# Optimization experiments

Hardware: AMD Instinct MI355X
Metric: run time of the kernel (lower is better)

## Reference

```python
import math
import jax, jax.numpy as jnp
import numpy as np

D_MODEL = 1024
D_HIDDEN = 2048
N_EXPERTS = 8
TOP_K = 2
CAPACITY_FACTOR = 1.25


def setup_inputs() -> dict:
    key = jax.random.key(0)
    k0, k1, k2, k3 = jax.random.split(key, 4)
    B, T = 2, 2048
    x = jax.random.normal(k0, (B, T, D_MODEL), dtype=jnp.float32)
    # torch nn.Linear stores weight as [out_features, in_features]
    w_router = jax.random.normal(k1, (N_EXPERTS, D_MODEL), dtype=jnp.float32) * 0.02
    w_gate = jax.random.normal(k2, (D_HIDDEN, D_MODEL), dtype=jnp.float32) * 0.02
    w_down = jax.random.normal(k3, (N_EXPERTS, D_MODEL, D_HIDDEN), dtype=jnp.float32) * 0.02
    return {"x": x, "w_router": w_router, "w_gate": w_gate, "w_down": w_down}


def _moe_forward(x, w_router, w_gate, w_down):
    B, T, D = x.shape
    N = B * T
    xf = x.reshape(N, D)

    # Router (computed in fp32, as in the original)
    logits = xf.astype(jnp.float32) @ w_router.T            # [N, E]
    gates = jax.nn.softmax(logits, axis=-1)                  # [N, E]
    topk_gates, topk_idx = jax.lax.top_k(gates, TOP_K)       # [N, K]

    # expert_mask[n, e] = 1 if expert e is among token n's top-k
    expert_mask = jax.nn.one_hot(topk_idx, N_EXPERTS, dtype=jnp.int32).sum(axis=1)  # [N, E]

    # Capacity masking via cumulative position within each expert's buffer
    capacity = math.ceil(N / N_EXPERTS * CAPACITY_FACTOR)
    position_in_expert = jnp.cumsum(expert_mask, axis=0) - 1
    expert_mask = expert_mask * (position_in_expert < capacity)

    keep = jnp.take_along_axis(expert_mask, topk_idx, axis=1) > 0  # [N, K]
    topk_gates = topk_gates * keep
    topk_gates = topk_gates / (topk_gates.sum(axis=-1, keepdims=True) + 1e-6)

    # Shared up-projection + SiLU (dropout = 0)
    hidden = jax.nn.silu(xf @ w_gate.T)                      # [N, H]

    # combine[n, e] = sum_k topk_gates[n, k] * [topk_idx[n, k] == e]
    combine = (topk_gates[:, :, None]
               * jax.nn.one_hot(topk_idx, N_EXPERTS, dtype=topk_gates.dtype)).sum(axis=1)  # [N, E]

    # Combine: y[n] = sum_e combine[n, e] * (hidden[n] @ w_down[e].T)
    # (dropped tokens have combine weight 0, matching the gated index_add in torch)
    y = jnp.zeros((N, D), dtype=x.dtype)
    for e in range(N_EXPERTS):  # small fixed loop over experts
        y = y + combine[:, e:e + 1] * (hidden @ w_down[e].T)
    return y.reshape(B, T, D)


def reference(x, w_router, w_gate, w_down):
    return _moe_forward(x, w_router, w_gate, w_down)
```

## Files before the change

### kernel.cpp

```cpp
#include <hip/hip_runtime.h>
#include <hip/hip_bf16.h>
#include <math.h>

#define NTOK 4096
#define DMODEL 1024
#define DHID 2048
#define NEXP 8
#define CAP 640

typedef __attribute__((ext_vector_type(8))) short short8;
typedef __attribute__((ext_vector_type(4))) float f32x4;

__device__ inline short f2bf(float f) {
    union { float f; unsigned u; } v; v.f = f;
    unsigned r = v.u + 0x7FFF + ((v.u >> 16) & 1);
    return (short)(r >> 16);
}

__device__ inline void async16(const short* g, short* l) {
    __builtin_amdgcn_global_load_lds(
        (const __attribute__((address_space(1))) unsigned*)g,
        (__attribute__((address_space(3))) unsigned*)l, 16, 0, 0);
}

__global__ __launch_bounds__(256) void router_kernel(
        const float* __restrict__ x, const float* __restrict__ wr, short* __restrict__ Xb,
        int2* __restrict__ topk_idx, float2* __restrict__ topk_gate)
{
    const int token = blockIdx.x * 4 + (threadIdx.x >> 6);
    const int lane  = threadIdx.x & 63;
    const float* xr = x + (size_t)token * DMODEL + lane * 16;
    float4 xv[4];
#pragma unroll
    for (int j = 0; j < 4; j++) xv[j] = ((const float4*)xr)[j];
    short8 s0 = { f2bf(xv[0].x), f2bf(xv[0].y), f2bf(xv[0].z), f2bf(xv[0].w),
                  f2bf(xv[1].x), f2bf(xv[1].y), f2bf(xv[1].z), f2bf(xv[1].w) };
    short8 s1 = { f2bf(xv[2].x), f2bf(xv[2].y), f2bf(xv[2].z), f2bf(xv[2].w),
                  f2bf(xv[3].x), f2bf(xv[3].y), f2bf(xv[3].z), f2bf(xv[3].w) };
    short* xo = Xb + (size_t)token * DMODEL + lane * 16;
    *(short8*)xo = s0;
    *(short8*)(xo + 8) = s1;

    float acc[NEXP];
#pragma unroll
    for (int e = 0; e < NEXP; e++) acc[e] = 0.f;
#pragma unroll
    for (int j = 0; j < 4; j++) {
#pragma unroll
        for (int e = 0; e < NEXP; e++) {
            float4 wv = ((const float4*)(wr + e * DMODEL + lane * 16))[j];
            acc[e] += xv[j].x * wv.x + xv[j].y * wv.y + xv[j].z * wv.z + xv[j].w * wv.w;
        }
    }
#pragma unroll
    for (int off = 32; off >= 1; off >>= 1) {
#pragma unroll
        for (int e = 0; e < NEXP; e++) acc[e] += __shfl_xor(acc[e], off, 64);
    }
    if (lane == 0) {
        float m = acc[0];
#pragma unroll
        for (int e = 1; e < NEXP; e++) m = fmaxf(m, acc[e]);
        float den = 0.f, g[NEXP];
#pragma unroll
        for (int e = 0; e < NEXP; e++) { g[e] = __expf(acc[e] - m); den += g[e]; }
        float inv = 1.f / den;
#pragma unroll
        for (int e = 0; e < NEXP; e++) g[e] *= inv;
        int i0 = 0; float l0 = acc[0];
#pragma unroll
        for (int e = 1; e < NEXP; e++) if (acc[e] > l0) { l0 = acc[e]; i0 = e; }
        int i1 = -1; float l1 = -1e30f;
#pragma unroll
        for (int e = 0; e < NEXP; e++) if (e != i0 && acc[e] > l1) { l1 = acc[e]; i1 = e; }
        topk_idx[token]  = make_int2(i0, i1);
        topk_gate[token] = make_float2(g[i0], g[i1]);
    }
}

__global__ __launch_bounds__(256) void router_fb_kernel(
        const float* __restrict__ x, const float* __restrict__ wr,
        int2* __restrict__ topk_idx, float2* __restrict__ topk_gate)
{
    const int token = blockIdx.x * 4 + (threadIdx.x >> 6);
    const int lane  = threadIdx.x & 63;
    const float* xr = x + (size_t)token * DMODEL + lane * 16;
    float acc[NEXP];
#pragma unroll
    for (int e = 0; e < NEXP; e++) acc[e] = 0.f;
#pragma unroll
    for (int j = 0; j < 4; j++) {
        float4 xv = ((const float4*)xr)[j];
#pragma unroll
        for (int e = 0; e < NEXP; e++) {
            float4 wv = ((const float4*)(wr + e * DMODEL + lane * 16))[j];
            acc[e] += xv.x * wv.x + xv.y * wv.y + xv.z * wv.z + xv.w * wv.w;
        }
    }
#pragma unroll
    for (int off = 32; off >= 1; off >>= 1) {
#pragma unroll
        for (int e = 0; e < NEXP; e++) acc[e] += __shfl_xor(acc[e], off, 64);
    }
    if (lane == 0) {
        float m = acc[0];
#pragma unroll
        for (int e = 1; e < NEXP; e++) m = fmaxf(m, acc[e]);
        float den = 0.f, g[NEXP];
#pragma unroll
        for (int e = 0; e < NEXP; e++) { g[e] = __expf(acc[e] - m); den += g[e]; }
        float inv = 1.f / den;
#pragma unroll
        for (int e = 0; e < NEXP; e++) g[e] *= inv;
        int i0 = 0; float l0 = acc[0];
#pragma unroll
        for (int e = 1; e < NEXP; e++) if (acc[e] > l0) { l0 = acc[e]; i0 = e; }
        int i1 = -1; float l1 = -1e30f;
#pragma unroll
        for (int e = 0; e < NEXP; e++) if (e != i0 && acc[e] > l1) { l1 = acc[e]; i1 = e; }
        topk_idx[token]  = make_int2(i0, i1);
        topk_gate[token] = make_float2(g[i0], g[i1]);
    }
}

__global__ __launch_bounds__(256) void convert_kernel(
        const float* __restrict__ src, short* __restrict__ dst)
{
    const size_t base = ((size_t)blockIdx.x * 256 + threadIdx.x) * 8;
    float4 a = ((const float4*)(src + base))[0];
    float4 b = ((const float4*)(src + base))[1];
    short8 s = { f2bf(a.x), f2bf(a.y), f2bf(a.z), f2bf(a.w),
                 f2bf(b.x), f2bf(b.y), f2bf(b.z), f2bf(b.w) };
    *(short8*)(dst + base) = s;
}

__global__ __launch_bounds__(1024) void scan_kernel(
        const int2* __restrict__ topk_idx, const float2* __restrict__ topk_gate,
        int* __restrict__ gtok, float* __restrict__ gw, int* __restrict__ gcnt)
{
    __shared__ unsigned long long wt0[16], wt1[16];
    const int th = threadIdx.x, lane = th & 63, wid = th >> 6;
    int2 idx[4]; float2 gt[4];
#pragma unroll
    for (int j = 0; j < 4; j++) { idx[j] = topk_idx[th * 4 + j]; gt[j] = topk_gate[th * 4 + j]; }
    unsigned long long c0 = 0, c1 = 0;
#pragma unroll
    for (int j = 0; j < 4; j++) {
        int e0 = idx[j].x, e1 = idx[j].y;
        if (e0 < 4) c0 += 1ull << (e0 * 16); else c1 += 1ull << ((e0 - 4) * 16);
        if (e1 < 4) c0 += 1ull << (e1 * 16); else c1 += 1ull << ((e1 - 4) * 16);
    }
    const unsigned long long my0 = c0, my1 = c1;
#pragma unroll
    for (int d = 1; d < 64; d <<= 1) {
        unsigned long long t0 = __shfl_up(c0, d, 64);
        unsigned long long t1 = __shfl_up(c1, d, 64);
        if (lane >= d) { c0 += t0; c1 += t1; }
    }
    if (lane == 63) { wt0[wid] = c0; wt1[wid] = c1; }
    __syncthreads();
    unsigned long long o0 = 0, o1 = 0;
    for (int w = 0; w < wid; w++) { o0 += wt0[w]; o1 += wt1[w]; }
    c0 += o0; c1 += o1;
    if (th == 1023) {
#pragma unroll
        for (int e = 0; e < 4; e++) gcnt[e]     = min((int)((c0 >> (e * 16)) & 0xFFFF), CAP);
#pragma unroll
        for (int e = 0; e < 4; e++) gcnt[4 + e] = min((int)((c1 >> (e * 16)) & 0xFFFF), CAP);
    }
    const unsigned long long x0 = c0 - my0, x1 = c1 - my1;
    int base[NEXP];
#pragma unroll
    for (int e = 0; e < 4; e++) base[e]     = (int)((x0 >> (e * 16)) & 0xFFFF);
#pragma unroll
    for (int e = 0; e < 4; e++) base[4 + e] = (int)((x1 >> (e * 16)) & 0xFFFF);
#pragma unroll
    for (int j = 0; j < 4; j++) {
        const int n = th * 4 + j;
        const int e0 = idx[j].x, e1 = idx[j].y;
        const int p0 = base[e0]++;
        const int p1 = base[e1]++;
        const bool k0 = p0 < CAP, k1 = p1 < CAP;
        const float gg0 = k0 ? gt[j].x : 0.f, gg1 = k1 ? gt[j].y : 0.f;
        const float invs = 1.f / (gg0 + gg1 + 1e-6f);
        if (k0) { gtok[e0 * CAP + p0] = n; gw[e0 * CAP + p0] = gg0 * invs; }
        if (k1) { gtok[e1 * CAP + p1] = n; gw[e1 * CAP + p1] = gg1 * invs; }
    }
}

__global__ __launch_bounds__(256) void gemm1_kernel(
        const short* __restrict__ Xb, const short* __restrict__ WGb, short* __restrict__ Hid)
{
    __shared__ __align__(16) short As[128 * 64];
    __shared__ __align__(16) short Bs[128 * 64];
    const int t = threadIdx.x;
    const int wave = t >> 6, lane = t & 63;
    const int m0 = blockIdx.y * 128, n0 = blockIdx.x * 128;
    const int wm = (wave >> 1) * 64, wn = (wave & 1) * 64;
    const int lm = lane & 15, lq = lane >> 4, lk = lq * 8;

    const short *ga[4], *gb[4];
    short *la[4], *lb[4];
#pragma unroll
    for (int j = 0; j < 4; j++) {
        const int c = j * 256 + t, r = c >> 3, col = (c & 7) * 8;
        la[j] = &As[c * 8]; lb[j] = &Bs[c * 8];
        ga[j] = Xb  + (size_t)(m0 + r) * DMODEL + col;
        gb[j] = WGb + (size_t)(n0 + r) * DMODEL + col;
    }

    f32x4 acc[4][4];
#pragma unroll
    for (int a = 0; a < 4; a++)
#pragma unroll
        for (int b = 0; b < 4; b++) acc[a][b] = (f32x4)(0.f);

    for (int k0 = 0; k0 < DMODEL; k0 += 64) {
#pragma unroll
        for (int j = 0; j < 4; j++) { async16(ga[j] + k0, la[j]); async16(gb[j] + k0, lb[j]); }
        __syncthreads();
#pragma unroll
        for (int kk = 0; kk < 64; kk += 32) {
            short8 af[4], bf[4];
#pragma unroll
            for (int mi = 0; mi < 4; mi++) af[mi] = *(const short8*)&As[(wm + mi * 16 + lm) * 64 + kk + lk];
#pragma unroll
            for (int ni = 0; ni < 4; ni++) bf[ni] = *(const short8*)&Bs[(wn + ni * 16 + lm) * 64 + kk + lk];
#pragma unroll
            for (int mi = 0; mi < 4; mi++)
#pragma unroll
                for (int ni = 0; ni < 4; ni++)
                    acc[mi][ni] = __builtin_amdgcn_mfma_f32_16x16x32_bf16(af[mi], bf[ni], acc[mi][ni], 0, 0, 0);
        }
        __syncthreads();
    }
#pragma unroll
    for (int mi = 0; mi < 4; mi++)
#pragma unroll
        for (int i = 0; i < 4; i++) {
            const int row = m0 + wm + mi * 16 + lq * 4 + i;
#pragma unroll
            for (int ni = 0; ni < 4; ni++) {
                const int col = n0 + wn + ni * 16 + lm;
                const float v = acc[mi][ni][i];
                const float s = v / (1.f + __expf(-v));
                Hid[(size_t)row * DHID + col] = f2bf(s);
            }
        }
}

__global__ __launch_bounds__(256) void gemm2_kernel(
        const short* __restrict__ Hid, const short* __restrict__ WDb,
        const int* __restrict__ gtok, const float* __restrict__ gw,
        const int* __restrict__ gcnt, float* __restrict__ Y)
{
    __shared__ __align__(16) short As[128 * 64];
    __shared__ __align__(16) short Bs[128 * 64];
    __shared__ int   tok_s[128];
    __shared__ float w_s[128];
    const int e  = blockIdx.x;
    const int n0 = blockIdx.y * 128;
    const int m0 = (blockIdx.z >> 1) * 128;
    const int ks = blockIdx.z & 1;
    const int cnt = gcnt[e];
    if (m0 >= cnt) return;
    const int t = threadIdx.x;
    const int wave = t >> 6, lane = t & 63;
    const int wm = (wave >> 1) * 64, wn = (wave & 1) * 64;
    const int lm = lane & 15, lq = lane >> 4, lk = lq * 8;
    const short* WDe = WDb + (size_t)e * DMODEL * DHID;

    if (t < 128) {
        const int r = m0 + t;
        const bool v = r < cnt;
        tok_s[t] = v ? gtok[e * CAP + r] : 0;
        w_s[t]   = v ? gw[e * CAP + r] : 0.f;
    }
    __syncthreads();

    const short *ga[4], *gb[4];
    short *la[4], *lb[4];
#pragma unroll
    for (int j = 0; j < 4; j++) {
        const int c = j * 256 + t, r = c >> 3, col = (c & 7) * 8;
        la[j] = &As[c * 8]; lb[j] = &Bs[c * 8];
        ga[j] = Hid + (size_t)tok_s[r] * DHID + col;
        gb[j] = WDe + (size_t)(n0 + r) * DHID + col;
    }

    f32x4 acc[4][4];
#pragma unroll
    for (int a = 0; a < 4; a++)
#pragma unroll
        for (int b = 0; b < 4; b++) acc[a][b] = (f32x4)(0.f);

    const int kbeg = ks * (DHID / 2), kend = kbeg + DHID / 2;
    for (int k0 = kbeg; k0 < kend; k0 += 64) {
#pragma unroll
        for (int j = 0; j < 4; j++) { async16(ga[j] + k0, la[j]); async16(gb[j] + k0, lb[j]); }
        __syncthreads();
#pragma unroll
        for (int kk = 0; kk < 64; kk += 32) {
            short8 af[4], bf[4];
#pragma unroll
            for (int mi = 0; mi < 4; mi++) af[mi] = *(const short8*)&As[(wm + mi * 16 + lm) * 64 + kk + lk];
#pragma unroll
            for (int ni = 0; ni < 4; ni++) bf[ni] = *(const short8*)&Bs[(wn + ni * 16 + lm) * 64 + kk + lk];
#pragma unroll
            for (int mi = 0; mi < 4; mi++)
#pragma unroll
                for (int ni = 0; ni < 4; ni++)
                    acc[mi][ni] = __builtin_amdgcn_mfma_f32_16x16x32_bf16(af[mi], bf[ni], acc[mi][ni], 0, 0, 0);
        }
        __syncthreads();
    }
#pragma unroll
    for (int mi = 0; mi < 4; mi++)
#pragma unroll
        for (int i = 0; i < 4; i++) {
            const int r = wm + mi * 16 + lq * 4 + i;
            const float wr = w_s[r];
            if (wr > 0.f) {
                const int token = tok_s[r];
#pragma unroll
                for (int ni = 0; ni < 4; ni++) {
                    const int col = n0 + wn + ni * 16 + lm;
                    atomicAdd(&Y[(size_t)token * DMODEL + col], acc[mi][ni][i] * wr);
                }
            }
        }
}

__global__ __launch_bounds__(256) void gemm1_fb_kernel(
        const float* __restrict__ X, const float* __restrict__ WG, short* __restrict__ Hid)
{
    __shared__ short As[128][72];
    __shared__ short Bs[128][72];
    const int t = threadIdx.x;
    const int wave = t >> 6, lane = t & 63;
    const int m0 = blockIdx.y * 128, n0 = blockIdx.x * 128;
    const int wm = (wave >> 1) * 64, wn = (wave & 1) * 64;
    const int lm = lane & 15, lq = lane >> 4, lk = lq * 8;
    const int r0 = t >> 3, c8 = (t & 7) * 8;

    f32x4 acc[4][4];
#pragma unroll
    for (int a = 0; a < 4; a++)
#pragma unroll
        for (int b = 0; b < 4; b++) acc[a][b] = (f32x4)(0.f);

    for (int k0 = 0; k0 < DMODEL; k0 += 64) {
#pragma unroll
        for (int i = 0; i < 4; i++) {
            const int row = r0 + i * 32;
            const float* ga = X + (size_t)(m0 + row) * DMODEL + k0 + c8;
            float4 v0 = ((const float4*)ga)[0];
            float4 v1 = ((const float4*)ga)[1];
            short8 s = { f2bf(v0.x), f2bf(v0.y), f2bf(v0.z), f2bf(v0.w),
                         f2bf(v1.x), f2bf(v1.y), f2bf(v1.z), f2bf(v1.w) };
            *(short8*)&As[row][c8] = s;
            const float* gb = WG + (size_t)(n0 + row) * DMODEL + k0 + c8;
            float4 w0 = ((const float4*)gb)[0];
            float4 w1 = ((const float4*)gb)[1];
            short8 sw = { f2bf(w0.x), f2bf(w0.y), f2bf(w0.z), f2bf(w0.w),
                          f2bf(w1.x), f2bf(w1.y), f2bf(w1.z), f2bf(w1.w) };
            *(short8*)&Bs[row][c8] = sw;
        }
        __syncthreads();
#pragma unroll
        for (int kk = 0; kk < 64; kk += 32) {
            short8 af[4], bf[4];
#pragma unroll
            for (int mi = 0; mi < 4; mi++) af[mi] = *(const short8*)&As[wm + mi * 16 + lm][kk + lk];
#pragma unroll
            for (int ni = 0; ni < 4; ni++) bf[ni] = *(const short8*)&Bs[wn + ni * 16 + lm][kk + lk];
#pragma unroll
            for (int mi = 0; mi < 4; mi++)
#pragma unroll
                for (int ni = 0; ni < 4; ni++)
                    acc[mi][ni] = __builtin_amdgcn_mfma_f32_16x16x32_bf16(af[mi], bf[ni], acc[mi][ni], 0, 0, 0);
        }
        __syncthreads();
    }
#pragma unroll
    for (int mi = 0; mi < 4; mi++)
#pragma unroll
        for (int i = 0; i < 4; i++) {
            const int row = m0 + wm + mi * 16 + lq * 4 + i;
#pragma unroll
            for (int ni = 0; ni < 4; ni++) {
                const int col = n0 + wn + ni * 16 + lm;
                const float v = acc[mi][ni][i];
                const float s = v / (1.f + __expf(-v));
                Hid[(size_t)row * DHID + col] = f2bf(s);
            }
        }
}

__global__ __launch_bounds__(256) void gemm2_fb_kernel(
        const short* __restrict__ Hid, const float* __restrict__ WD,
        const int* __restrict__ gtok, const float* __restrict__ gw,
        const int* __restrict__ gcnt, float* __restrict__ Y)
{
    __shared__ short As[128][72];
    __shared__ short Bs[128][72];
    __shared__ int   tok_s[128];
    __shared__ float w_s[128];
    const int e = blockIdx.z;
    const int cnt = gcnt[e];
    const int m0 = blockIdx.y * 128;
    if (m0 >= cnt) return;
    const int n0 = blockIdx.x * 128;
    const int t = threadIdx.x;
    const int wave = t >> 6, lane = t & 63;
    const int wm = (wave >> 1) * 64, wn = (wave & 1) * 64;
    const int lm = lane & 15, lq = lane >> 4, lk = lq * 8;
    const int r0 = t >> 3, c8 = (t & 7) * 8;
    const float* WDe = WD + (size_t)e * DMODEL * DHID;

    if (t < 128) {
        const int r = m0 + t;
        const bool v = r < cnt;
        tok_s[t] = v ? gtok[e * CAP + r] : 0;
        w_s[t]   = v ? gw[e * CAP + r] : 0.f;
    }
    __syncthreads();

    f32x4 acc[4][4];
#pragma unroll
    for (int a = 0; a < 4; a++)
#pragma unroll
        for (int b = 0; b < 4; b++) acc[a][b] = (f32x4)(0.f);

    const int tokA[4] = { tok_s[r0], tok_s[r0 + 32], tok_s[r0 + 64], tok_s[r0 + 96] };

    for (int k0 = 0; k0 < DHID; k0 += 64) {
#pragma unroll
        for (int i = 0; i < 4; i++) {
            const int row = r0 + i * 32;
            uint4 av = *(const uint4*)(Hid + (size_t)tokA[i] * DHID + k0 + c8);
            *(uint4*)&As[row][c8] = av;
            const float* gb = WDe + (size_t)(n0 + row) * DHID + k0 + c8;
            float4 w0 = ((const float4*)gb)[0];
            float4 w1 = ((const float4*)gb)[1];
            short8 sw = { f2bf(w0.x), f2bf(w0.y), f2bf(w0.z), f2bf(w0.w),
                          f2bf(w1.x), f2bf(w1.y), f2bf(w1.z), f2bf(w1.w) };
            *(short8*)&Bs[row][c8] = sw;
        }
        __syncthreads();
#pragma unroll
        for (int kk = 0; kk < 64; kk += 32) {
            short8 af[4], bf[4];
#pragma unroll
            for (int mi = 0; mi < 4; mi++) af[mi] = *(const short8*)&As[wm + mi * 16 + lm][kk + lk];
#pragma unroll
            for (int ni = 0; ni < 4; ni++) bf[ni] = *(const short8*)&Bs[wn + ni * 16 + lm][kk + lk];
#pragma unroll
            for (int mi = 0; mi < 4; mi++)
#pragma unroll
                for (int ni = 0; ni < 4; ni++)
                    acc[mi][ni] = __builtin_amdgcn_mfma_f32_16x16x32_bf16(af[mi], bf[ni], acc[mi][ni], 0, 0, 0);
        }
        __syncthreads();
    }
#pragma unroll
    for (int mi = 0; mi < 4; mi++)
#pragma unroll
        for (int i = 0; i < 4; i++) {
            const int r = wm + mi * 16 + lq * 4 + i;
            const float wr = w_s[r];
            if (wr > 0.f) {
                const int token = tok_s[r];
#pragma unroll
                for (int ni = 0; ni < 4; ni++) {
                    const int col = n0 + wn + ni * 16 + lm;
                    atomicAdd(&Y[(size_t)token * DMODEL + col], acc[mi][ni][i] * wr);
                }
            }
        }
}

extern "C" void kernel_launch(void* const* d_in, const int* in_sizes, int n_in,
                              void* d_out, int out_size, void* d_ws, size_t ws_size,
                              hipStream_t stream) {
    const float* x  = (const float*)d_in[0];
    const float* wr = (const float*)d_in[1];
    const float* wg = (const float*)d_in[2];
    const float* wd = (const float*)d_in[3];
    float* y = (float*)d_out;

    char* w = (char*)d_ws;
    int2*   topk_idx  = (int2*)w;    w += NTOK * sizeof(int2);
    float2* topk_gate = (float2*)w;  w += NTOK * sizeof(float2);
    int*    gtok      = (int*)w;     w += NEXP * CAP * sizeof(int);
    float*  gw        = (float*)w;   w += NEXP * CAP * sizeof(float);
    int*    gcnt      = (int*)w;     w += 256;
    short*  Hid       = (short*)w;   w += (size_t)NTOK * DHID * sizeof(short);
    short*  Xb        = (short*)w;   w += (size_t)NTOK * DMODEL * sizeof(short);
    short*  WGb       = (short*)w;   w += (size_t)DHID * DMODEL * sizeof(short);
    short*  WDb       = (short*)w;   w += (size_t)NEXP * DMODEL * DHID * sizeof(short);
    const size_t need_full = (size_t)(w - (char*)d_ws);

    hipMemsetAsync(y, 0, (size_t)NTOK * DMODEL * sizeof(float), stream);

    if (ws_size >= need_full) {
        router_kernel<<<NTOK / 4, 256, 0, stream>>>(x, wr, Xb, topk_idx, topk_gate);
        convert_kernel<<<(DHID * DMODEL) / (256 * 8), 256, 0, stream>>>(wg, WGb);
        convert_kernel<<<(NEXP * DMODEL * DHID) / (256 * 8), 256, 0, stream>>>(wd, WDb);
        scan_kernel<<<1, 1024, 0, stream>>>(topk_idx, topk_gate, gtok, gw, gcnt);
        gemm1_kernel<<<dim3(DHID / 128, NTOK / 128), 256, 0, stream>>>(Xb, WGb, Hid);
        gemm2_kernel<<<dim3(NEXP, DMODEL / 128, 2 * ((CAP + 127) / 128)), 256, 0, stream>>>(
            Hid, WDb, gtok, gw, gcnt, y);
    } else {
        router_fb_kernel<<<NTOK / 4, 256, 0, stream>>>(x, wr, topk_idx, topk_gate);
        scan_kernel<<<1, 1024, 0, stream>>>(topk_idx, topk_gate, gtok, gw, gcnt);
        gemm1_fb_kernel<<<dim3(DHID / 128, NTOK / 128), 256, 0, stream>>>(x, wg, Hid);
        gemm2_fb_kernel<<<dim3(DMODEL / 128, (CAP + 127) / 128, NEXP), 256, 0, stream>>>(
            Hid, wd, gtok, gw, gcnt, y);
    }
}
```

Baseline: 248.9 us.

## Replace atomic split-K expert GEMM with slot outputs, gather combine, fragment-ordered LDS

The expert GEMM no longer splits K and scatters atomicAdd results into Y. Each expert tile now writes unweighted bf16 outputs to a per-slot buffer, and a new combine kernel gathers each token's two slots and applies the normalized gates. This removes the output memset and the fp32 atomics. Both GEMMs also stage tiles in LDS in MFMA-fragment order so each lane reads contiguous 16 bytes, which is meant to avoid bank conflicts. The cost is an extra kernel, an extra bf16 round-trip of the expert outputs with added rounding error, and less parallelism in gemm2 now that split-K is gone.

```diff
diff --git a/kernel.cpp b/kernel.cpp
--- a/kernel.cpp
+++ b/kernel.cpp
@@ -16,7 +16,9 @@
     unsigned r = v.u + 0x7FFF + ((v.u >> 16) & 1);
     return (short)(r >> 16);
 }
-
+__device__ inline float bf2f(unsigned short u) {
+    union { unsigned u; float f; } v; v.u = ((unsigned)u) << 16; return v.f;
+}
 __device__ inline void async16(const short* g, short* l) {
     __builtin_amdgcn_global_load_lds(
         (const __attribute__((address_space(1))) unsigned*)g,
@@ -136,7 +138,8 @@
 
 __global__ __launch_bounds__(1024) void scan_kernel(
         const int2* __restrict__ topk_idx, const float2* __restrict__ topk_gate,
-        int* __restrict__ gtok, float* __restrict__ gw, int* __restrict__ gcnt)
+        int* __restrict__ gtok, float* __restrict__ gw, int* __restrict__ gcnt,
+        int2* __restrict__ tslot, float2* __restrict__ tw)
 {
     __shared__ unsigned long long wt0[16], wt1[16];
     const int th = threadIdx.x, lane = th & 63, wid = th >> 6;
@@ -183,8 +186,12 @@
         const bool k0 = p0 < CAP, k1 = p1 < CAP;
         const float gg0 = k0 ? gt[j].x : 0.f, gg1 = k1 ? gt[j].y : 0.f;
         const float invs = 1.f / (gg0 + gg1 + 1e-6f);
-        if (k0) { gtok[e0 * CAP + p0] = n; gw[e0 * CAP + p0] = gg0 * invs; }
-        if (k1) { gtok[e1 * CAP + p1] = n; gw[e1 * CAP + p1] = gg1 * invs; }
+        const int s0 = k0 ? e0 * CAP + p0 : 0;
+        const int s1 = k1 ? e1 * CAP + p1 : 0;
+        if (k0) { gtok[s0] = n; gw[s0] = gg0 * invs; }
+        if (k1) { gtok[s1] = n; gw[s1] = gg1 * invs; }
+        tslot[n] = make_int2(s0, s1);
+        tw[n]    = make_float2(gg0 * invs, gg1 * invs);
     }
 }
 
@@ -197,16 +204,19 @@
     const int wave = t >> 6, lane = t & 63;
     const int m0 = blockIdx.y * 128, n0 = blockIdx.x * 128;
     const int wm = (wave >> 1) * 64, wn = (wave & 1) * 64;
-    const int lm = lane & 15, lq = lane >> 4, lk = lq * 8;
+    const int lm = lane & 15, lq = lane >> 4;
 
     const short *ga[4], *gb[4];
     short *la[4], *lb[4];
 #pragma unroll
     for (int j = 0; j < 4; j++) {
-        const int c = j * 256 + t, r = c >> 3, col = (c & 7) * 8;
-        la[j] = &As[c * 8]; lb[j] = &Bs[c * 8];
-        ga[j] = Xb  + (size_t)(m0 + r) * DMODEL + col;
-        gb[j] = WGb + (size_t)(n0 + r) * DMODEL + col;
+        const int b   = wave * 4 + j;
+        const int row = (b >> 1) * 16 + lm;
+        const int col = (b & 1) * 32 + lq * 8;
+        la[j] = &As[b * 512 + lane * 8];
+        lb[j] = &Bs[b * 512 + lane * 8];
+        ga[j] = Xb  + (size_t)(m0 + row) * DMODEL + col;
+        gb[j] = WGb + (size_t)(n0 + row) * DMODEL + col;
     }
 
     f32x4 acc[4][4];
@@ -220,12 +230,14 @@
         for (int j = 0; j < 4; j++) { async16(ga[j] + k0, la[j]); async16(gb[j] + k0, lb[j]); }
         __syncthreads();
 #pragma unroll
-        for (int kk = 0; kk < 64; kk += 32) {
+        for (int kk = 0; kk < 2; kk++) {
             short8 af[4], bf[4];
 #pragma unroll
-            for (int mi = 0; mi < 4; mi++) af[mi] = *(const short8*)&As[(wm + mi * 16 + lm) * 64 + kk + lk];
-#pragma unroll
-            for (int ni = 0; ni < 4; ni++) bf[ni] = *(const short8*)&Bs[(wn + ni * 16 + lm) * 64 + kk + lk];
+            for (int mi = 0; mi < 4; mi++)
+                af[mi] = *(const short8*)&As[((((wm >> 4) + mi) * 2 + kk) * 64 + lane) * 8];
+#pragma unroll
+            for (int ni = 0; ni < 4; ni++)
+                bf[ni] = *(const short8*)&Bs[((((wn >> 4) + ni) * 2 + kk) * 64 + lane) * 8];
 #pragma unroll
             for (int mi = 0; mi < 4; mi++)
 #pragma unroll
@@ -251,30 +263,26 @@
 
 __global__ __launch_bounds__(256) void gemm2_kernel(
         const short* __restrict__ Hid, const short* __restrict__ WDb,
-        const int* __restrict__ gtok, const float* __restrict__ gw,
-        const int* __restrict__ gcnt, float* __restrict__ Y)
+        const int* __restrict__ gtok, const int* __restrict__ gcnt,
+        short* __restrict__ Yp)
 {
     __shared__ __align__(16) short As[128 * 64];
     __shared__ __align__(16) short Bs[128 * 64];
-    __shared__ int   tok_s[128];
-    __shared__ float w_s[128];
+    __shared__ int tok_s[128];
     const int e  = blockIdx.x;
     const int n0 = blockIdx.y * 128;
-    const int m0 = (blockIdx.z >> 1) * 128;
-    const int ks = blockIdx.z & 1;
+    const int m0 = blockIdx.z * 128;
     const int cnt = gcnt[e];
     if (m0 >= cnt) return;
     const int t = threadIdx.x;
     const int wave = t >> 6, lane = t & 63;
     const int wm = (wave >> 1) * 64, wn = (wave & 1) * 64;
-    const int lm = lane & 15, lq = lane >> 4, lk = lq * 8;
+    const int lm = lane & 15, lq = lane >> 4;
     const short* WDe = WDb + (size_t)e * DMODEL * DHID;
 
     if (t < 128) {
         const int r = m0 + t;
-        const bool v = r < cnt;
-        tok_s[t] = v ? gtok[e * CAP + r] : 0;
-        w_s[t]   = v ? gw[e * CAP + r] : 0.f;
+        tok_s[t] = (r < cnt) ? gtok[e * CAP + r] : 0;
     }
     __syncthreads();
 
@@ -282,10 +290,13 @@
     short *la[4], *lb[4];
 #pragma unroll
     for (int j = 0; j < 4; j++) {
-        const int c = j * 256 + t, r = c >> 3, col = (c & 7) * 8;
-        la[j] = &As[c * 8]; lb[j] = &Bs[c * 8];
-        ga[j] = Hid + (size_t)tok_s[r] * DHID + col;
-        gb[j] = WDe + (size_t)(n0 + r) * DHID + col;
+        const int b   = wave * 4 + j;
+        const int row = (b >> 1) * 16 + lm;
+        const int col = (b & 1) * 32 + lq * 8;
+        la[j] = &As[b * 512 + lane * 8];
+        lb[j] = &Bs[b * 512 + lane * 8];
+        ga[j] = Hid + (size_t)tok_s[row] * DHID + col;
+        gb[j] = WDe + (size_t)(n0 + row) * DHID + col;
     }
 
     f32x4 acc[4][4];
@@ -294,18 +305,19 @@
 #pragma unroll
         for (int b = 0; b < 4; b++) acc[a][b] = (f32x4)(0.f);
 
-    const int kbeg = ks * (DHID / 2), kend = kbeg + DHID / 2;
-    for (int k0 = kbeg; k0 < kend; k0 += 64) {
+    for (int k0 = 0; k0 < DHID; k0 += 64) {
 #pragma unroll
         for (int j = 0; j < 4; j++) { async16(ga[j] + k0, la[j]); async16(gb[j] + k0, lb[j]); }
         __syncthreads();
 #pragma unroll
-        for (int kk = 0; kk < 64; kk += 32) {
+        for (int kk = 0; kk < 2; kk++) {
             short8 af[4], bf[4];
 #pragma unroll
-            for (int mi = 0; mi < 4; mi++) af[mi] = *(const short8*)&As[(wm + mi * 16 + lm) * 64 + kk + lk];
-#pragma unroll
-            for (int ni = 0; ni < 4; ni++) bf[ni] = *(const short8*)&Bs[(wn + ni * 16 + lm) * 64 + kk + lk];
+            for (int mi = 0; mi < 4; mi++)
+                af[mi] = *(const short8*)&As[((((wm >> 4) + mi) * 2 + kk) * 64 + lane) * 8];
+#pragma unroll
+            for (int ni = 0; ni < 4; ni++)
+                bf[ni] = *(const short8*)&Bs[((((wn >> 4) + ni) * 2 + kk) * 64 + lane) * 8];
 #pragma unroll
             for (int mi = 0; mi < 4; mi++)
 #pragma unroll
@@ -318,17 +330,31 @@
     for (int mi = 0; mi < 4; mi++)
 #pragma unroll
         for (int i = 0; i < 4; i++) {
-            const int r = wm + mi * 16 + lq * 4 + i;
-            const float wr = w_s[r];
-            if (wr > 0.f) {
-                const int token = tok_s[r];
-#pragma unroll
-                for (int ni = 0; ni < 4; ni++) {
-                    const int col = n0 + wn + ni * 16 + lm;
-                    atomicAdd(&Y[(size_t)token * DMODEL + col], acc[mi][ni][i] * wr);
-                }
+            const int slot = e * CAP + m0 + wm + mi * 16 + lq * 4 + i;
+#pragma unroll
+            for (int ni = 0; ni < 4; ni++) {
+                const int col = n0 + wn + ni * 16 + lm;
+                Yp[(size_t)slot * DMODEL + col] = f2bf(acc[mi][ni][i]);
             }
         }
+}
+
+__global__ __launch_bounds__(256) void combine_kernel(
+        const short* __restrict__ Yp, const int2* __restrict__ tslot,
+        const float2* __restrict__ tw, float* __restrict__ y)
+{
+    const int token = blockIdx.x;
+    const int c = threadIdx.x * 4;
+    const int2   s = tslot[token];
+    const float2 w = tw[token];
+    ushort4 a = *(const ushort4*)((const unsigned short*)Yp + (size_t)s.x * DMODEL + c);
+    ushort4 b = *(const ushort4*)((const unsigned short*)Yp + (size_t)s.y * DMODEL + c);
+    float4 o;
+    o.x = w.x * bf2f(a.x) + w.y * bf2f(b.x);
+    o.y = w.x * bf2f(a.y) + w.y * bf2f(b.y);
+    o.z = w.x * bf2f(a.z) + w.y * bf2f(b.z);
+    o.w = w.x * bf2f(a.w) + w.y * bf2f(b.w);
+    *(float4*)&y[(size_t)token * DMODEL + c] = o;
 }
 
 __global__ __launch_bounds__(256) void gemm1_fb_kernel(
@@ -495,25 +521,29 @@
     int*    gtok      = (int*)w;     w += NEXP * CAP * sizeof(int);
     float*  gw        = (float*)w;   w += NEXP * CAP * sizeof(float);
     int*    gcnt      = (int*)w;     w += 256;
+    int2*   tslot     = (int2*)w;    w += NTOK * sizeof(int2);
+    float2* tw        = (float2*)w;  w += NTOK * sizeof(float2);
     short*  Hid       = (short*)w;   w += (size_t)NTOK * DHID * sizeof(short);
-    short*  Xb        = (short*)w;   w += (size_t)NTOK * DMODEL * sizeof(short);
-    short*  WGb       = (short*)w;   w += (size_t)DHID * DMODEL * sizeof(short);
     short*  WDb       = (short*)w;   w += (size_t)NEXP * DMODEL * DHID * sizeof(short);
+    short*  Xb        = (short*)w;
+    short*  WGb       = (short*)(w + (size_t)NTOK * DMODEL * sizeof(short));
+    short*  Yp        = (short*)w;
+    w += (size_t)NTOK * DMODEL * sizeof(short) + (size_t)DHID * DMODEL * sizeof(short);
     const size_t need_full = (size_t)(w - (char*)d_ws);
-
-    hipMemsetAsync(y, 0, (size_t)NTOK * DMODEL * sizeof(float), stream);
 
     if (ws_size >= need_full) {
         router_kernel<<<NTOK / 4, 256, 0, stream>>>(x, wr, Xb, topk_idx, topk_gate);
         convert_kernel<<<(DHID * DMODEL) / (256 * 8), 256, 0, stream>>>(wg, WGb);
+        scan_kernel<<<1, 1024, 0, stream>>>(topk_idx, topk_gate, gtok, gw, gcnt, tslot, tw);
+        gemm1_kernel<<<dim3(DHID / 128, NTOK / 128), 256, 0, stream>>>(Xb, WGb, Hid);
         convert_kernel<<<(NEXP * DMODEL * DHID) / (256 * 8), 256, 0, stream>>>(wd, WDb);
-        scan_kernel<<<1, 1024, 0, stream>>>(topk_idx, topk_gate, gtok, gw, gcnt);
-        gemm1_kernel<<<dim3(DHID / 128, NTOK / 128), 256, 0, stream>>>(Xb, WGb, Hid);
-        gemm2_kernel<<<dim3(NEXP, DMODEL / 128, 2 * ((CAP + 127) / 128)), 256, 0, stream>>>(
-            Hid, WDb, gtok, gw, gcnt, y);
+        gemm2_kernel<<<dim3(NEXP, DMODEL / 128, CAP / 128), 256, 0, stream>>>(
+            Hid, WDb, gtok, gcnt, Yp);
+        combine_kernel<<<NTOK, 256, 0, stream>>>(Yp, tslot, tw, y);
     } else {
+        hipMemsetAsync(y, 0, (size_t)NTOK * DMODEL * sizeof(float), stream);
         router_fb_kernel<<<NTOK / 4, 256, 0, stream>>>(x, wr, topk_idx, topk_gate);
-        scan_kernel<<<1, 1024, 0, stream>>>(topk_idx, topk_gate, gtok, gw, gcnt);
+        scan_kernel<<<1, 1024, 0, stream>>>(topk_idx, topk_gate, gtok, gw, gcnt, tslot, tw);
         gemm1_fb_kernel<<<dim3(DHID / 128, NTOK / 128), 256, 0, stream>>>(x, wg, Hid);
         gemm2_fb_kernel<<<dim3(DMODEL / 128, (CAP + 127) / 128, NEXP), 256, 0, stream>>>(
             Hid, wd, gtok, gw, gcnt, y);
```

Measured after the change: 247.9 us. Within noise of the previous version (-0.4%).
